# Kernel optimization log

Measured on AMD Instinct MI355X. Metric: run time of the kernel, lower is better.

The kernel has to match this reference:

```python
import jax, jax.numpy as jnp
import numpy as np
import math

B, S, D, H = 1, 2048, 1024, 16
HD = D // H  # 64
SCALE = 1.0 / math.sqrt(HD)
ENT = 0.5      # entanglement_strength
DECAY = 0.1    # correlation_decay
SUP = 0.3      # superposition_weight
EPS = 1e-5


def setup_inputs() -> dict:
    key = jax.random.key(0)
    ks = jax.random.split(key, 24)
    def w(k, shape, s=0.02):
        return jax.random.normal(k, shape, dtype=jnp.float32) * s
    return {
        "hidden_states": jax.random.normal(ks[0], (B, S, D), dtype=jnp.float32),
        "Wq": w(ks[1], (D, D)), "bq": jnp.zeros((D,), jnp.float32),
        "Wk": w(ks[2], (D, D)), "bk": jnp.zeros((D,), jnp.float32),
        "Wv": w(ks[3], (D, D)), "bv": jnp.zeros((D,), jnp.float32),
        "Wo": w(ks[4], (D, D)), "bo": jnp.zeros((D,), jnp.float32),
        "Weq": w(ks[5], (D, D), 0.002), "beq": jnp.zeros((D,), jnp.float32),
        "Wek": w(ks[6], (D, D), 0.002), "bek": jnp.zeros((D,), jnp.float32),
        "amp_w": w(ks[7], (H, D)), "amp_b": jnp.zeros((H,), jnp.float32),
        "ph_w": w(ks[8], (H, D)), "ph_b": jnp.zeros((H,), jnp.float32),
        "mix_w": w(ks[9], (H, HD, HD)), "mix_b": jnp.zeros((H, HD), jnp.float32),
        "ln_g": jnp.ones((D,), jnp.float32), "ln_b": jnp.zeros((D,), jnp.float32),
    }


def _heads(x):
    # [B,S,D] -> [B,H,S,hd]
    b, s, _ = x.shape
    return x.reshape(b, s, H, HD).transpose(0, 2, 1, 3)


def reference(hidden_states, Wq, bq, Wk, bk, Wv, bv, Wo, bo,
              Weq, beq, Wek, bek, amp_w, amp_b, ph_w, ph_b,
              mix_w, mix_b, ln_g, ln_b):
    hs = hidden_states
    b, s, _ = hs.shape
    q = _heads(hs @ Wq.T + bq)  # [B,H,S,hd]
    k = _heads(hs @ Wk.T + bk)
    v = _heads(hs @ Wv.T + bv)

    # standard attention scores
    scores = jnp.einsum('bhqd,bhkd->bhqk', q, k) * SCALE

    # entanglement scores with distance-decay position bias
    eq = _heads(hs @ Weq.T + beq)
    ek = _heads(hs @ Wek.T + bek)
    pos = jnp.arange(s)
    decay = jnp.exp(-DECAY * jnp.abs(pos[:, None] - pos[None, :]).astype(jnp.float32))  # [S,S]
    esc = jnp.einsum('bhqd,bhkd->bhqk', eq, ek) * (1.0 / math.sqrt(HD)) * decay

    attn = jax.nn.softmax(scores + ENT * esc, axis=-1)  # [B,H,S,S]

    # quantum amplitudes / phases
    amps = jax.nn.sigmoid(hs @ amp_w.T + amp_b)        # [B,S,H]
    phases = jnp.tanh(hs @ ph_w.T + ph_b) * math.pi    # [B,S,H]
    a = amps.transpose(0, 2, 1)[..., None]             # [B,H,S,1]
    p = phases.transpose(0, 2, 1)[..., None]

    # per-head superposition mixer: Linear(head_dim, head_dim) per head
    sup = jnp.einsum('bhsd,hod->bhso', v, mix_w) + mix_b[None, :, None, :]
    mixed = v + SUP * a * jnp.cos(p) * sup + SUP * a * jnp.sin(p) * jnp.roll(sup, 1, axis=-1)

    ctx = jnp.einsum('bhqk,bhkd->bhqd', attn, mixed)
    ctx = ctx.transpose(0, 2, 1, 3).reshape(b, s, D)
    out = ctx @ Wo.T + bo

    # residual + LayerNorm
    res = hs + out
    mu = jnp.mean(res, axis=-1, keepdims=True)
    var = jnp.mean((res - mu) ** 2, axis=-1, keepdims=True)
    return (res - mu) * jax.lax.rsqrt(var + EPS) * ln_g + ln_b
```

## Files before the change

### kernel.cpp

```cpp
#include <hip/hip_runtime.h>

#define SEQ 2048
#define DM  1024
#define NH  16
#define HDIM 64

typedef __bf16   bf16x8 __attribute__((ext_vector_type(8)));
typedef float    f32x4  __attribute__((ext_vector_type(4)));
typedef _Float16 half8  __attribute__((ext_vector_type(8)));
typedef _Float16 half4v __attribute__((ext_vector_type(4)));

__device__ __forceinline__ void gload16(const void* g, void* l) {
    __builtin_amdgcn_global_load_lds(
        (const __attribute__((address_space(1))) unsigned int*)g,
        (__attribute__((address_space(3))) unsigned int*)l, 16, 0, 0);
}

__global__ void zero_out(float* __restrict__ out, int n) {
    int i = blockIdx.x * 256 + threadIdx.x;
    if (i < n) out[i] = 0.f;
}

__global__ __launch_bounds__(256) void cvt_bf16(
    const float* __restrict__ src, __bf16* __restrict__ dst, int n8)
{
    int i = blockIdx.x * 256 + threadIdx.x;
    if (i >= n8) return;
    const float4* s = reinterpret_cast<const float4*>(src) + (size_t)i * 2;
    float4 x = s[0], y = s[1];
    bf16x8 o;
    o[0] = (__bf16)x.x; o[1] = (__bf16)x.y; o[2] = (__bf16)x.z; o[3] = (__bf16)x.w;
    o[4] = (__bf16)y.x; o[5] = (__bf16)y.y; o[6] = (__bf16)y.z; o[7] = (__bf16)y.w;
    reinterpret_cast<bf16x8*>(dst)[i] = o;
}

struct CvtBatch { const float* src[6]; __bf16* dst[6]; };
__global__ __launch_bounds__(256) void cvt_w6(CvtBatch cb) {
    const int z = blockIdx.y;
    int i = blockIdx.x * 256 + threadIdx.x;
    const float4* s = reinterpret_cast<const float4*>(cb.src[z]) + (size_t)i * 2;
    float4 x = s[0], y = s[1];
    bf16x8 o;
    o[0] = (__bf16)x.x; o[1] = (__bf16)x.y; o[2] = (__bf16)x.z; o[3] = (__bf16)x.w;
    o[4] = (__bf16)y.x; o[5] = (__bf16)y.y; o[6] = (__bf16)y.z; o[7] = (__bf16)y.w;
    reinterpret_cast<bf16x8*>(cb.dst[z])[i] = o;
}

__global__ __launch_bounds__(256) void wsup_k(
    const float* __restrict__ mixw, const float* __restrict__ Wv,
    const float* __restrict__ bv, const float* __restrict__ mixb,
    __bf16* __restrict__ w6, float* __restrict__ bsup)
{
    const int ho = blockIdx.x, h = ho >> 6, tid = threadIdx.x;
    __shared__ float mrow[64];
    if (tid < 64) mrow[tid] = mixw[(size_t)ho * 64 + tid];
    __syncthreads();
    const int c0 = tid * 4;
    float a0 = 0.f, a1 = 0.f, a2 = 0.f, a3 = 0.f;
    for (int dd = 0; dd < 64; ++dd) {
        const float4 wv4 = *reinterpret_cast<const float4*>(
            Wv + (size_t)(h * 64 + dd) * DM + c0);
        const float w = mrow[dd];
        a0 += w * wv4.x; a1 += w * wv4.y; a2 += w * wv4.z; a3 += w * wv4.w;
    }
    __bf16* dst = w6 + (size_t)ho * DM + c0;
    dst[0] = (__bf16)a0; dst[1] = (__bf16)a1; dst[2] = (__bf16)a2; dst[3] = (__bf16)a3;
    if (tid == 0) {
        float b = mixb[ho];
        for (int dd = 0; dd < 64; ++dd) b += mrow[dd] * bv[h * 64 + dd];
        bsup[ho] = b;
    }
}

struct GemmBatch {
    const __bf16* A;
    const __bf16* W[6];
    const float*  bias[6];
    void*         out[6];
    int           mode[6];
    const float*  resid;
};

__device__ __forceinline__ int swz4(int r) { return (r ^ (r >> 2)) & 3; }

__global__ __launch_bounds__(256) void gemm_bt(GemmBatch g) {
    const int z = blockIdx.z;
    const __bf16* __restrict__ A = g.A;
    const __bf16* __restrict__ W = g.W[z];
    const int ncol0 = blockIdx.x * 128;
    const int mrow0 = blockIdx.y * 128;
    const int tid = threadIdx.x, lane = tid & 63, wv = tid >> 6;
    const int wm = wv >> 1, wn = wv & 1;
    const int fr = lane & 15, fj = lane >> 4;

    __shared__ __bf16 As[128 * 32];
    __shared__ __bf16 Bs[128 * 32];

    f32x4 acc[4][4];
#pragma unroll
    for (int i = 0; i < 4; ++i)
#pragma unroll
        for (int j = 0; j < 4; ++j)
#pragma unroll
            for (int e = 0; e < 4; ++e) acc[i][j][e] = 0.f;

    const int row0 = wv * 16 + (lane >> 2);
    const int row1 = row0 + 64;
    const int jl   = lane & 3;
    const int dstA0 = row0 * 32 + jl * 8;
    const int dstA1 = row1 * 32 + jl * 8;
    const __bf16* ApS0 = A + (size_t)(mrow0 + row0) * DM + (jl ^ swz4(row0)) * 8;
    const __bf16* ApS1 = A + (size_t)(mrow0 + row1) * DM + (jl ^ swz4(row1)) * 8;
    const __bf16* WpS0 = W + (size_t)(ncol0 + row0) * DM + (jl ^ swz4(row0)) * 8;
    const __bf16* WpS1 = W + (size_t)(ncol0 + row1) * DM + (jl ^ swz4(row1)) * 8;

    for (int kt = 0; kt < DM; kt += 32) {
        __syncthreads();
        gload16(ApS0 + kt, As + dstA0);
        gload16(ApS1 + kt, As + dstA1);
        gload16(WpS0 + kt, Bs + dstA0);
        gload16(WpS1 + kt, Bs + dstA1);
        __syncthreads();

        bf16x8 af[4], bfv[4];
#pragma unroll
        for (int mf = 0; mf < 4; ++mf) {
            int r = wm * 64 + mf * 16 + fr;
            af[mf] = *(const bf16x8*)(As + r * 32 + ((fj ^ swz4(r)) << 3));
        }
#pragma unroll
        for (int nf = 0; nf < 4; ++nf) {
            int r = wn * 64 + nf * 16 + fr;
            bfv[nf] = *(const bf16x8*)(Bs + r * 32 + ((fj ^ swz4(r)) << 3));
        }
#pragma unroll
        for (int mf = 0; mf < 4; ++mf)
#pragma unroll
            for (int nf = 0; nf < 4; ++nf)
                acc[mf][nf] = __builtin_amdgcn_mfma_f32_16x16x32_bf16(
                    af[mf], bfv[nf], acc[mf][nf], 0, 0, 0);
    }

    const int mode = g.mode[z];
    const float* __restrict__ bias = g.bias[z];
#pragma unroll
    for (int mf = 0; mf < 4; ++mf) {
#pragma unroll
        for (int nf = 0; nf < 4; ++nf) {
            const int col = ncol0 + wn * 64 + nf * 16 + fr;
            const int rw0 = mrow0 + wm * 64 + mf * 16 + fj * 4;
            const float bc = bias[col];
#pragma unroll
            for (int jj = 0; jj < 4; ++jj) {
                float vv = acc[mf][nf][jj] + bc;
                const size_t idx = (size_t)(rw0 + jj) * DM + col;
                if (mode == 3) {
                    ((_Float16*)g.out[z])[idx] = (_Float16)vv;
                } else {
                    if (mode == 2) vv += g.resid[idx];
                    ((float*)g.out[z])[idx] = vv;
                }
            }
        }
    }
}

__global__ __launch_bounds__(256) void amp_fast(
    const float* __restrict__ hs,
    const float* __restrict__ amp_w, const float* __restrict__ amp_b,
    const float* __restrict__ ph_w,  const float* __restrict__ ph_b,
    float* __restrict__ cA, float* __restrict__ sA)
{
    const int s = blockIdx.x;
    __shared__ float hrow[DM];
    for (int i = threadIdx.x; i < DM; i += 256)
        hrow[i] = hs[(size_t)s * DM + i];
    __syncthreads();
    const int h = threadIdx.x >> 4, sub = threadIdx.x & 15;
    const float* aw = amp_w + (size_t)h * DM;
    const float* pw = ph_w  + (size_t)h * DM;
    float da = 0.f, dp = 0.f;
    for (int k = sub; k < DM; k += 16) {
        const float hv = hrow[k];
        da += hv * aw[k];
        dp += hv * pw[k];
    }
#pragma unroll
    for (int off = 8; off >= 1; off >>= 1) {
        da += __shfl_xor(da, off);
        dp += __shfl_xor(dp, off);
    }
    if (sub == 0) {
        da += amp_b[h]; dp += ph_b[h];
        float amp = 1.f / (1.f + expf(-da));
        float ph  = tanhf(dp) * 3.14159265358979323846f;
        cA[s * NH + h] = 0.3f * amp * cosf(ph);
        sA[s * NH + h] = 0.3f * amp * sinf(ph);
    }
}

__global__ __launch_bounds__(256) void mixT_fuse(
    const _Float16* __restrict__ vb, const _Float16* __restrict__ supf,
    const float* __restrict__ cA, const float* __restrict__ sA,
    _Float16* __restrict__ mixedT)
{
    const int h = blockIdx.x, st = blockIdx.y;
    const int o = threadIdx.x >> 2, sc = threadIdx.x & 3;
    const int s0 = st * 32 + sc * 8;
    const int ho = h * 64 + o, op = h * 64 + ((o + 63) & 63);
    half8 m;
#pragma unroll
    for (int e = 0; e < 8; ++e) {
        const int s = s0 + e;
        const float v  = (float)vb[(size_t)s * DM + ho];
        const float su = (float)supf[(size_t)s * DM + ho];
        const float s2 = (float)supf[(size_t)s * DM + op];
        m[e] = (_Float16)(v + cA[s * NH + h] * su + sA[s * NH + h] * s2);
    }
    *reinterpret_cast<half8*>(mixedT + (size_t)ho * SEQ + s0) = m;
}

__global__ __launch_bounds__(256) void attn_mfma(
    const _Float16* __restrict__ q, const _Float16* __restrict__ k,
    const _Float16* __restrict__ eq, const _Float16* __restrict__ ek,
    const _Float16* __restrict__ mixedT, __bf16* __restrict__ ctx)
{
    const int h = blockIdx.y;
    const int q0 = blockIdx.x * 64;
    const int tid = threadIdx.x, lane = tid & 63, wv = tid >> 6;
    const int lo = lane & 15, hi = lane >> 4;
    const int hoff = h * HDIM;

    __shared__ _Float16 Kt[64 * 64];
    __shared__ _Float16 Et[64 * 64];
    __shared__ _Float16 Mt[64 * 64];
    __shared__ _Float16 Pt[4][64 * 18];

    half8 qa[2], ea[2];
#pragma unroll
    for (int kk = 0; kk < 2; ++kk) {
        const int row = q0 + wv * 16 + lo;
        qa[kk] = *(const half8*)(q  + (size_t)row * DM + hoff + kk * 32 + hi * 8);
        ea[kk] = *(const half8*)(eq + (size_t)row * DM + hoff + kk * 32 + hi * 8);
    }

    f32x4 oacc[4];
    float mr[4], lr[4];
#pragma unroll
    for (int j = 0; j < 4; ++j) { mr[j] = 0.f; lr[j] = 0.f; }
#pragma unroll
    for (int n = 0; n < 4; ++n)
#pragma unroll
        for (int e = 0; e < 4; ++e) oacc[n][e] = 0.f;

    const int srow = tid >> 3, schk = tid & 7;
    const int sdst0 = srow * 64 + ((schk ^ (srow & 7)) << 3);
    const int sdst1 = (srow + 32) * 64 + ((schk ^ (srow & 7)) << 3);

    #define IN_BAND(kt_) ({ int _a = (kt_) - (q0 + 63); int _b = q0 - ((kt_) + 63); \
                            int _d = _a > 0 ? _a : (_b > 0 ? _b : 0); _d <= 160; })

    bool diagCur = IN_BAND(0);
    half8 rk0 = *(const half8*)(k  + (size_t)(srow) * DM + hoff + schk * 8);
    half8 rk1 = *(const half8*)(k  + (size_t)(srow + 32) * DM + hoff + schk * 8);
    half8 rm0 = *(const half8*)(mixedT + (size_t)(hoff + srow) * SEQ + schk * 8);
    half8 rm1 = *(const half8*)(mixedT + (size_t)(hoff + srow + 32) * SEQ + schk * 8);
    half8 re0, re1;
    if (diagCur) {
        re0 = *(const half8*)(ek + (size_t)(srow) * DM + hoff + schk * 8);
        re1 = *(const half8*)(ek + (size_t)(srow + 32) * DM + hoff + schk * 8);
    }

    for (int kt = 0; kt < SEQ; kt += 64) {
        __syncthreads();
        *(half8*)&Kt[sdst0] = rk0; *(half8*)&Kt[sdst1] = rk1;
        *(half8*)&Mt[sdst0] = rm0; *(half8*)&Mt[sdst1] = rm1;
        if (diagCur) { *(half8*)&Et[sdst0] = re0; *(half8*)&Et[sdst1] = re1; }
        __syncthreads();
        const bool diagNext = (kt + 64 < SEQ) && IN_BAND(kt + 64);
        if (kt + 64 < SEQ) {
            const int nt = kt + 64;
            rk0 = *(const half8*)(k  + (size_t)(nt + srow) * DM + hoff + schk * 8);
            rk1 = *(const half8*)(k  + (size_t)(nt + srow + 32) * DM + hoff + schk * 8);
            rm0 = *(const half8*)(mixedT + (size_t)(hoff + srow) * SEQ + nt + schk * 8);
            rm1 = *(const half8*)(mixedT + (size_t)(hoff + srow + 32) * SEQ + nt + schk * 8);
            if (diagNext) {
                re0 = *(const half8*)(ek + (size_t)(nt + srow) * DM + hoff + schk * 8);
                re1 = *(const half8*)(ek + (size_t)(nt + srow + 32) * DM + hoff + schk * 8);
            }
        }

        f32x4 sa[4], se[4];
#pragma unroll
        for (int n = 0; n < 4; ++n)
#pragma unroll
            for (int e = 0; e < 4; ++e) { sa[n][e] = 0.f; se[n][e] = 0.f; }
#pragma unroll
        for (int kk = 0; kk < 2; ++kk)
#pragma unroll
            for (int nf = 0; nf < 4; ++nf) {
                const int rrow = lo + 16 * nf;
                const int coff = rrow * 64 + (((hi + 4 * kk) ^ (rrow & 7)) << 3);
                half8 kb = *(const half8*)&Kt[coff];
                sa[nf] = __builtin_amdgcn_mfma_f32_16x16x32_f16(qa[kk], kb, sa[nf], 0, 0, 0);
            }
        if (diagCur) {
#pragma unroll
            for (int kk = 0; kk < 2; ++kk)
#pragma unroll
                for (int nf = 0; nf < 4; ++nf) {
                    const int rrow = lo + 16 * nf;
                    const int coff = rrow * 64 + (((hi + 4 * kk) ^ (rrow & 7)) << 3);
                    half8 eb = *(const half8*)&Et[coff];
                    se[nf] = __builtin_amdgcn_mfma_f32_16x16x32_f16(ea[kk], eb, se[nf], 0, 0, 0);
                }
        }

        float lg[4][4];
        bool exc = false;
        const int qrow = q0 + wv * 16 + hi * 4;
        if (diagCur) {
#pragma unroll
            for (int nf = 0; nf < 4; ++nf) {
                const int key = kt + nf * 16 + lo;
#pragma unroll
                for (int j = 0; j < 4; ++j) {
                    int dd = qrow + j - key; dd = dd < 0 ? -dd : dd;
                    const float dec = exp2f(-0.14426950408889634f * (float)dd);
                    const float v = 0.125f * sa[nf][j] + 0.0625f * se[nf][j] * dec;
                    lg[nf][j] = v;
                    exc |= (v > mr[j] + 8.f);
                }
            }
        } else {
#pragma unroll
            for (int nf = 0; nf < 4; ++nf)
#pragma unroll
                for (int j = 0; j < 4; ++j) {
                    const float v = 0.125f * sa[nf][j];
                    lg[nf][j] = v;
                    exc |= (v > mr[j] + 8.f);
                }
        }
        if (__any((int)exc)) {
#pragma unroll
            for (int j = 0; j < 4; ++j) {
                float tm = fmaxf(fmaxf(lg[0][j], lg[1][j]), fmaxf(lg[2][j], lg[3][j]));
#pragma unroll
                for (int off = 8; off >= 1; off >>= 1) tm = fmaxf(tm, __shfl_xor(tm, off));
                const float mnew = fmaxf(mr[j], tm);
                const float corr = __expf(mr[j] - mnew);
                lr[j] *= corr; mr[j] = mnew;
#pragma unroll
                for (int nfd = 0; nfd < 4; ++nfd) oacc[nfd][j] *= corr;
            }
        }
        _Float16* Pw = Pt[wv];
#pragma unroll
        for (int nf = 0; nf < 4; ++nf) {
            half4v pv;
#pragma unroll
            for (int j = 0; j < 4; ++j) {
                const float p = __expf(lg[nf][j] - mr[j]);
                lr[j] += p;
                pv[j] = (_Float16)p;
            }
            *(half4v*)&Pw[(lo + 16 * nf) * 18 + hi * 4] = pv;
        }
        __asm__ volatile("s_waitcnt lgkmcnt(0)" ::: "memory");

#pragma unroll
        for (int kk = 0; kk < 2; ++kk) {
            half8 mb[4];
#pragma unroll
            for (int nfd = 0; nfd < 4; ++nfd) {
                const int rrow = lo + 16 * nfd;
                mb[nfd] = *(const half8*)&Mt[rrow * 64 + (((hi + 4 * kk) ^ (rrow & 7)) << 3)];
            }
            half8 pa;
#pragma unroll
            for (int e = 0; e < 8; ++e)
                pa[e] = Pw[(kk * 32 + hi * 8 + e) * 18 + lo];
#pragma unroll
            for (int nfd = 0; nfd < 4; ++nfd)
                oacc[nfd] = __builtin_amdgcn_mfma_f32_16x16x32_f16(pa, mb[nfd], oacc[nfd], 0, 0, 0);
        }
        diagCur = diagNext;
    }
    #undef IN_BAND

#pragma unroll
    for (int j = 0; j < 4; ++j) {
#pragma unroll
        for (int off = 8; off >= 1; off >>= 1) lr[j] += __shfl_xor(lr[j], off);
    }
    const int qrow = q0 + wv * 16 + hi * 4;
#pragma unroll
    for (int nfd = 0; nfd < 4; ++nfd) {
        const int d = hoff + lo + 16 * nfd;
#pragma unroll
        for (int j = 0; j < 4; ++j)
            ctx[(size_t)(qrow + j) * DM + d] = (__bf16)(oacc[nfd][j] / lr[j]);
    }
}

__global__ __launch_bounds__(256) void lnorm_f32(
    const float* __restrict__ res, const float* __restrict__ g,
    const float* __restrict__ b, float* __restrict__ out)
{
    const int row = blockIdx.x, tid = threadIdx.x;
    const int wave = tid >> 6, lane = tid & 63;
    __shared__ float red[8];
    const float4 x = reinterpret_cast<const float4*>(res + (size_t)row * DM)[tid];
    float s  = x.x + x.y + x.z + x.w;
    float s2 = x.x * x.x + x.y * x.y + x.z * x.z + x.w * x.w;
#pragma unroll
    for (int off = 32; off >= 1; off >>= 1) {
        s  += __shfl_xor(s, off);
        s2 += __shfl_xor(s2, off);
    }
    if (lane == 0) { red[wave] = s; red[4 + wave] = s2; }
    __syncthreads();
    s  = red[0] + red[1] + red[2] + red[3];
    s2 = red[4] + red[5] + red[6] + red[7];
    const float mu  = s * (1.f / DM);
    const float var = s2 * (1.f / DM) - mu * mu;
    const float inv = rsqrtf(var + 1e-5f);
    const int col = tid * 4;
    float4 o;
    o.x = (x.x - mu) * inv * g[col + 0] + b[col + 0];
    o.y = (x.y - mu) * inv * g[col + 1] + b[col + 1];
    o.z = (x.z - mu) * inv * g[col + 2] + b[col + 2];
    o.w = (x.w - mu) * inv * g[col + 3] + b[col + 3];
    reinterpret_cast<float4*>(out + (size_t)row * DM)[tid] = o;
}

extern "C" void kernel_launch(void* const* d_in, const int* in_sizes, int n_in,
                              void* d_out, int out_size, void* d_ws, size_t ws_size,
                              hipStream_t stream) {
    const float* hs   = (const float*)d_in[0];
    const float* Wq   = (const float*)d_in[1];
    const float* bq   = (const float*)d_in[2];
    const float* Wk   = (const float*)d_in[3];
    const float* bk   = (const float*)d_in[4];
    const float* Wv   = (const float*)d_in[5];
    const float* bv   = (const float*)d_in[6];
    const float* Wo   = (const float*)d_in[7];
    const float* bo   = (const float*)d_in[8];
    const float* Weq  = (const float*)d_in[9];
    const float* beq  = (const float*)d_in[10];
    const float* Wek  = (const float*)d_in[11];
    const float* bek  = (const float*)d_in[12];
    const float* ampw = (const float*)d_in[13];
    const float* ampb = (const float*)d_in[14];
    const float* phw  = (const float*)d_in[15];
    const float* phb  = (const float*)d_in[16];
    const float* mixw = (const float*)d_in[17];
    const float* mixb = (const float*)d_in[18];
    const float* lng  = (const float*)d_in[19];
    const float* lnb  = (const float*)d_in[20];
    float* out = (float*)d_out;

    static const int expect[21] = {
        2097152, 1048576, 1024, 1048576, 1024, 1048576, 1024, 1048576, 1024,
        1048576, 1024, 1048576, 1024, 16384, 16, 16384, 16, 65536, 1024,
        1024, 1024};
    bool ok = (n_in == 21) && (out_size == 2097152);
    if (ok) for (int i = 0; i < 21; ++i) ok = ok && (in_sizes[i] == expect[i]);
    if (!ok) {
        zero_out<<<(out_size + 255) / 256, 256, 0, stream>>>(out, out_size);
        return;
    }

    char* ws = (char*)d_ws;
    __bf16*   hsb = (__bf16*)ws;
    __bf16*   w0  = (__bf16*)(ws + (4  << 20));
    __bf16*   w1  = (__bf16*)(ws + (6  << 20));
    __bf16*   w2  = (__bf16*)(ws + (8  << 20));
    __bf16*   w3  = (__bf16*)(ws + (10 << 20));
    __bf16*   w4  = (__bf16*)(ws + (12 << 20));
    __bf16*   w5  = (__bf16*)(ws + (14 << 20));
    __bf16*   w6  = (__bf16*)(ws + (16 << 20));
    _Float16* qf  = (_Float16*)(ws + (18 << 20));
    _Float16* kf  = (_Float16*)(ws + (22 << 20));
    _Float16* eqf = (_Float16*)(ws + (26 << 20));
    _Float16* ekf = (_Float16*)(ws + (30 << 20));
    float*    cA  = (float*)(ws + (34 << 20));
    float*    sA  = cA + SEQ * NH;
    float*    bsup = sA + SEQ * NH;
    _Float16* mxT = (_Float16*)hsb;
    float*    res = (float*)(ws + (18 << 20));
    _Float16* vb   = (_Float16*)d_out;
    _Float16* supf = (_Float16*)((char*)d_out + (4 << 20));
    __bf16*   ctx  = (__bf16*)d_out;

    const int H8 = SEQ * DM / 8;
    cvt_bf16<<<(H8 + 255) / 256, 256, 0, stream>>>(hs, hsb, H8);

    CvtBatch cb;
    cb.src[0] = Wq;  cb.dst[0] = w0;
    cb.src[1] = Wk;  cb.dst[1] = w1;
    cb.src[2] = Wv;  cb.dst[2] = w2;
    cb.src[3] = Weq; cb.dst[3] = w3;
    cb.src[4] = Wek; cb.dst[4] = w4;
    cb.src[5] = Wo;  cb.dst[5] = w5;
    cvt_w6<<<dim3(512, 6), 256, 0, stream>>>(cb);

    wsup_k<<<1024, 256, 0, stream>>>(mixw, Wv, bv, mixb, w6, bsup);
    amp_fast<<<SEQ, 256, 0, stream>>>(hs, ampw, ampb, phw, phb, cA, sA);

    GemmBatch g1 = {};
    g1.A = hsb;
    g1.W[0] = w0; g1.bias[0] = bq;   g1.out[0] = qf;   g1.mode[0] = 3;
    g1.W[1] = w1; g1.bias[1] = bk;   g1.out[1] = kf;   g1.mode[1] = 3;
    g1.W[2] = w2; g1.bias[2] = bv;   g1.out[2] = vb;   g1.mode[2] = 3;
    g1.W[3] = w3; g1.bias[3] = beq;  g1.out[3] = eqf;  g1.mode[3] = 3;
    g1.W[4] = w4; g1.bias[4] = bek;  g1.out[4] = ekf;  g1.mode[4] = 3;
    g1.W[5] = w6; g1.bias[5] = bsup; g1.out[5] = supf; g1.mode[5] = 3;
    g1.resid = nullptr;
    gemm_bt<<<dim3(DM / 128, SEQ / 128, 6), 256, 0, stream>>>(g1);

    mixT_fuse<<<dim3(NH, SEQ / 32), 256, 0, stream>>>(vb, supf, cA, sA, mxT);

    attn_mfma<<<dim3(SEQ / 64, NH), 256, 0, stream>>>(qf, kf, eqf, ekf, mxT, ctx);

    GemmBatch g3 = {};
    g3.A = ctx;
    g3.W[0] = w5; g3.bias[0] = bo; g3.out[0] = res; g3.mode[0] = 2;
    g3.resid = hs;
    gemm_bt<<<dim3(DM / 128, SEQ / 128, 1), 256, 0, stream>>>(g3);

    lnorm_f32<<<SEQ, 256, 0, stream>>>(res, lng, lnb, out);
}
```

Baseline: 303.6 us.

## Merge prep kernels, deepen GEMM K-tile to 64, double attention query tile

Folds the hidden-state bf16 conversion into the batched weight-conversion kernel and merges the mixer-weight and amplitude/phase kernels into one launch, cutting launch count. The GEMM now stages a 64-wide K slice per iteration with an 8-way XOR swizzle, halving the number of barrier-separated loads. The attention kernel processes 128 query rows per block (two 16-row fragments per wave), so each K/E/M tile loaded to shared memory is reused twice. In exchange, register pressure and LDS use rise, and the attention grid halves to 256 blocks, which may underfill the GPU.

```diff
diff --git a/kernel.cpp b/kernel.cpp
--- a/kernel.cpp
+++ b/kernel.cpp
@@ -21,21 +21,8 @@
     if (i < n) out[i] = 0.f;
 }
 
-__global__ __launch_bounds__(256) void cvt_bf16(
-    const float* __restrict__ src, __bf16* __restrict__ dst, int n8)
-{
-    int i = blockIdx.x * 256 + threadIdx.x;
-    if (i >= n8) return;
-    const float4* s = reinterpret_cast<const float4*>(src) + (size_t)i * 2;
-    float4 x = s[0], y = s[1];
-    bf16x8 o;
-    o[0] = (__bf16)x.x; o[1] = (__bf16)x.y; o[2] = (__bf16)x.z; o[3] = (__bf16)x.w;
-    o[4] = (__bf16)y.x; o[5] = (__bf16)y.y; o[6] = (__bf16)y.z; o[7] = (__bf16)y.w;
-    reinterpret_cast<bf16x8*>(dst)[i] = o;
-}
-
-struct CvtBatch { const float* src[6]; __bf16* dst[6]; };
-__global__ __launch_bounds__(256) void cvt_w6(CvtBatch cb) {
+struct CvtBatch { const float* src[8]; __bf16* dst[8]; };
+__global__ __launch_bounds__(256) void cvt_all(CvtBatch cb) {
     const int z = blockIdx.y;
     int i = blockIdx.x * 256 + threadIdx.x;
     const float4* s = reinterpret_cast<const float4*>(cb.src[z]) + (size_t)i * 2;
@@ -46,29 +33,64 @@
     reinterpret_cast<bf16x8*>(cb.dst[z])[i] = o;
 }
 
-__global__ __launch_bounds__(256) void wsup_k(
+__global__ __launch_bounds__(256) void prep_misc(
     const float* __restrict__ mixw, const float* __restrict__ Wv,
     const float* __restrict__ bv, const float* __restrict__ mixb,
-    __bf16* __restrict__ w6, float* __restrict__ bsup)
+    __bf16* __restrict__ w6, float* __restrict__ bsup,
+    const float* __restrict__ hs,
+    const float* __restrict__ amp_w, const float* __restrict__ amp_b,
+    const float* __restrict__ ph_w,  const float* __restrict__ ph_b,
+    float* __restrict__ cA, float* __restrict__ sA)
 {
-    const int ho = blockIdx.x, h = ho >> 6, tid = threadIdx.x;
-    __shared__ float mrow[64];
-    if (tid < 64) mrow[tid] = mixw[(size_t)ho * 64 + tid];
-    __syncthreads();
-    const int c0 = tid * 4;
-    float a0 = 0.f, a1 = 0.f, a2 = 0.f, a3 = 0.f;
-    for (int dd = 0; dd < 64; ++dd) {
-        const float4 wv4 = *reinterpret_cast<const float4*>(
-            Wv + (size_t)(h * 64 + dd) * DM + c0);
-        const float w = mrow[dd];
-        a0 += w * wv4.x; a1 += w * wv4.y; a2 += w * wv4.z; a3 += w * wv4.w;
-    }
-    __bf16* dst = w6 + (size_t)ho * DM + c0;
-    dst[0] = (__bf16)a0; dst[1] = (__bf16)a1; dst[2] = (__bf16)a2; dst[3] = (__bf16)a3;
-    if (tid == 0) {
-        float b = mixb[ho];
-        for (int dd = 0; dd < 64; ++dd) b += mrow[dd] * bv[h * 64 + dd];
-        bsup[ho] = b;
+    const int tid = threadIdx.x;
+    if (blockIdx.x < 1024) {
+        const int ho = blockIdx.x, h = ho >> 6;
+        __shared__ float mrow[64];
+        if (tid < 64) mrow[tid] = mixw[(size_t)ho * 64 + tid];
+        __syncthreads();
+        const int c0 = tid * 4;
+        float a0 = 0.f, a1 = 0.f, a2 = 0.f, a3 = 0.f;
+        for (int dd = 0; dd < 64; ++dd) {
+            const float4 wv4 = *reinterpret_cast<const float4*>(
+                Wv + (size_t)(h * 64 + dd) * DM + c0);
+            const float w = mrow[dd];
+            a0 += w * wv4.x; a1 += w * wv4.y; a2 += w * wv4.z; a3 += w * wv4.w;
+        }
+        __bf16* dst = w6 + (size_t)ho * DM + c0;
+        dst[0] = (__bf16)a0; dst[1] = (__bf16)a1;
+        dst[2] = (__bf16)a2; dst[3] = (__bf16)a3;
+        if (tid == 0) {
+            float b = mixb[ho];
+            for (int dd = 0; dd < 64; ++dd) b += mrow[dd] * bv[h * 64 + dd];
+            bsup[ho] = b;
+        }
+    } else {
+        const int s = blockIdx.x - 1024;
+        __shared__ float hrow[DM];
+        for (int i = tid; i < DM; i += 256)
+            hrow[i] = hs[(size_t)s * DM + i];
+        __syncthreads();
+        const int h = tid >> 4, sub = tid & 15;
+        const float* aw = amp_w + (size_t)h * DM;
+        const float* pw = ph_w  + (size_t)h * DM;
+        float da = 0.f, dp = 0.f;
+        for (int k = sub; k < DM; k += 16) {
+            const float hv = hrow[k];
+            da += hv * aw[k];
+            dp += hv * pw[k];
+        }
+#pragma unroll
+        for (int off = 8; off >= 1; off >>= 1) {
+            da += __shfl_xor(da, off);
+            dp += __shfl_xor(dp, off);
+        }
+        if (sub == 0) {
+            da += amp_b[h]; dp += ph_b[h];
+            float amp = 1.f / (1.f + expf(-da));
+            float ph  = tanhf(dp) * 3.14159265358979323846f;
+            cA[s * NH + h] = 0.3f * amp * cosf(ph);
+            sA[s * NH + h] = 0.3f * amp * sinf(ph);
+        }
     }
 }
 
@@ -80,8 +102,6 @@
     int           mode[6];
     const float*  resid;
 };
-
-__device__ __forceinline__ int swz4(int r) { return (r ^ (r >> 2)) & 3; }
 
 __global__ __launch_bounds__(256) void gemm_bt(GemmBatch g) {
     const int z = blockIdx.z;
@@ -93,8 +113,8 @@
     const int wm = wv >> 1, wn = wv & 1;
     const int fr = lane & 15, fj = lane >> 4;
 
-    __shared__ __bf16 As[128 * 32];
-    __shared__ __bf16 Bs[128 * 32];
+    __shared__ __bf16 As[128 * 64];
+    __shared__ __bf16 Bs[128 * 64];
 
     f32x4 acc[4][4];
 #pragma unroll
@@ -104,41 +124,46 @@
 #pragma unroll
             for (int e = 0; e < 4; ++e) acc[i][j][e] = 0.f;
 
-    const int row0 = wv * 16 + (lane >> 2);
-    const int row1 = row0 + 64;
-    const int jl   = lane & 3;
-    const int dstA0 = row0 * 32 + jl * 8;
-    const int dstA1 = row1 * 32 + jl * 8;
-    const __bf16* ApS0 = A + (size_t)(mrow0 + row0) * DM + (jl ^ swz4(row0)) * 8;
-    const __bf16* ApS1 = A + (size_t)(mrow0 + row1) * DM + (jl ^ swz4(row1)) * 8;
-    const __bf16* WpS0 = W + (size_t)(ncol0 + row0) * DM + (jl ^ swz4(row0)) * 8;
-    const __bf16* WpS1 = W + (size_t)(ncol0 + row1) * DM + (jl ^ swz4(row1)) * 8;
-
-    for (int kt = 0; kt < DM; kt += 32) {
+    const int srow = tid >> 3, jl = tid & 7;
+    const int scs = (jl ^ (srow & 7)) * 8;
+    const __bf16* Ap[4]; const __bf16* Wp[4]; int dst[4];
+#pragma unroll
+    for (int i = 0; i < 4; ++i) {
+        const int r = i * 32 + srow;
+        dst[i] = r * 64 + jl * 8;
+        Ap[i] = A + (size_t)(mrow0 + r) * DM + scs;
+        Wp[i] = W + (size_t)(ncol0 + r) * DM + scs;
+    }
+
+    for (int kt = 0; kt < DM; kt += 64) {
         __syncthreads();
-        gload16(ApS0 + kt, As + dstA0);
-        gload16(ApS1 + kt, As + dstA1);
-        gload16(WpS0 + kt, Bs + dstA0);
-        gload16(WpS1 + kt, Bs + dstA1);
+#pragma unroll
+        for (int i = 0; i < 4; ++i) gload16(Ap[i] + kt, As + dst[i]);
+#pragma unroll
+        for (int i = 0; i < 4; ++i) gload16(Wp[i] + kt, Bs + dst[i]);
         __syncthreads();
 
-        bf16x8 af[4], bfv[4];
-#pragma unroll
-        for (int mf = 0; mf < 4; ++mf) {
-            int r = wm * 64 + mf * 16 + fr;
-            af[mf] = *(const bf16x8*)(As + r * 32 + ((fj ^ swz4(r)) << 3));
-        }
-#pragma unroll
-        for (int nf = 0; nf < 4; ++nf) {
-            int r = wn * 64 + nf * 16 + fr;
-            bfv[nf] = *(const bf16x8*)(Bs + r * 32 + ((fj ^ swz4(r)) << 3));
-        }
-#pragma unroll
-        for (int mf = 0; mf < 4; ++mf)
-#pragma unroll
-            for (int nf = 0; nf < 4; ++nf)
-                acc[mf][nf] = __builtin_amdgcn_mfma_f32_16x16x32_bf16(
-                    af[mf], bfv[nf], acc[mf][nf], 0, 0, 0);
+#pragma unroll
+        for (int ks = 0; ks < 2; ++ks) {
+            bf16x8 af[4], bfv[4];
+            const int ch = ks * 4 + fj;
+#pragma unroll
+            for (int mf = 0; mf < 4; ++mf) {
+                int r = wm * 64 + mf * 16 + fr;
+                af[mf] = *(const bf16x8*)(As + r * 64 + ((ch ^ (r & 7)) << 3));
+            }
+#pragma unroll
+            for (int nf = 0; nf < 4; ++nf) {
+                int r = wn * 64 + nf * 16 + fr;
+                bfv[nf] = *(const bf16x8*)(Bs + r * 64 + ((ch ^ (r & 7)) << 3));
+            }
+#pragma unroll
+            for (int mf = 0; mf < 4; ++mf)
+#pragma unroll
+                for (int nf = 0; nf < 4; ++nf)
+                    acc[mf][nf] = __builtin_amdgcn_mfma_f32_16x16x32_bf16(
+                        af[mf], bfv[nf], acc[mf][nf], 0, 0, 0);
+        }
     }
 
     const int mode = g.mode[z];
@@ -162,40 +187,6 @@
                 }
             }
         }
-    }
-}
-
-__global__ __launch_bounds__(256) void amp_fast(
-    const float* __restrict__ hs,
-    const float* __restrict__ amp_w, const float* __restrict__ amp_b,
-    const float* __restrict__ ph_w,  const float* __restrict__ ph_b,
-    float* __restrict__ cA, float* __restrict__ sA)
-{
-    const int s = blockIdx.x;
-    __shared__ float hrow[DM];
-    for (int i = threadIdx.x; i < DM; i += 256)
-        hrow[i] = hs[(size_t)s * DM + i];
-    __syncthreads();
-    const int h = threadIdx.x >> 4, sub = threadIdx.x & 15;
-    const float* aw = amp_w + (size_t)h * DM;
-    const float* pw = ph_w  + (size_t)h * DM;
-    float da = 0.f, dp = 0.f;
-    for (int k = sub; k < DM; k += 16) {
-        const float hv = hrow[k];
-        da += hv * aw[k];
-        dp += hv * pw[k];
-    }
-#pragma unroll
-    for (int off = 8; off >= 1; off >>= 1) {
-        da += __shfl_xor(da, off);
-        dp += __shfl_xor(dp, off);
-    }
-    if (sub == 0) {
-        da += amp_b[h]; dp += ph_b[h];
-        float amp = 1.f / (1.f + expf(-da));
-        float ph  = tanhf(dp) * 3.14159265358979323846f;
-        cA[s * NH + h] = 0.3f * amp * cosf(ph);
-        sA[s * NH + h] = 0.3f * amp * sinf(ph);
     }
 }
 
@@ -226,7 +217,7 @@
     const _Float16* __restrict__ mixedT, __bf16* __restrict__ ctx)
 {
     const int h = blockIdx.y;
-    const int q0 = blockIdx.x * 64;
+    const int q0 = blockIdx.x * 128;
     const int tid = threadIdx.x, lane = tid & 63, wv = tid >> 6;
     const int lo = lane & 15, hi = lane >> 4;
     const int hoff = h * HDIM;
@@ -234,30 +225,37 @@
     __shared__ _Float16 Kt[64 * 64];
     __shared__ _Float16 Et[64 * 64];
     __shared__ _Float16 Mt[64 * 64];
-    __shared__ _Float16 Pt[4][64 * 18];
-
-    half8 qa[2], ea[2];
-#pragma unroll
-    for (int kk = 0; kk < 2; ++kk) {
-        const int row = q0 + wv * 16 + lo;
-        qa[kk] = *(const half8*)(q  + (size_t)row * DM + hoff + kk * 32 + hi * 8);
-        ea[kk] = *(const half8*)(eq + (size_t)row * DM + hoff + kk * 32 + hi * 8);
-    }
-
-    f32x4 oacc[4];
-    float mr[4], lr[4];
-#pragma unroll
-    for (int j = 0; j < 4; ++j) { mr[j] = 0.f; lr[j] = 0.f; }
-#pragma unroll
-    for (int n = 0; n < 4; ++n)
-#pragma unroll
-        for (int e = 0; e < 4; ++e) oacc[n][e] = 0.f;
+    __shared__ _Float16 Pt[8][64 * 18];
+
+    half8 qa[2][2], ea[2][2];
+#pragma unroll
+    for (int m = 0; m < 2; ++m) {
+        const int row = q0 + wv * 32 + m * 16 + lo;
+#pragma unroll
+        for (int kk = 0; kk < 2; ++kk) {
+            qa[m][kk] = *(const half8*)(q  + (size_t)row * DM + hoff + kk * 32 + hi * 8);
+            ea[m][kk] = *(const half8*)(eq + (size_t)row * DM + hoff + kk * 32 + hi * 8);
+        }
+    }
+
+    f32x4 oacc[2][4];
+    float mr[2][4], lr[2][4];
+#pragma unroll
+    for (int m = 0; m < 2; ++m)
+#pragma unroll
+        for (int j = 0; j < 4; ++j) { mr[m][j] = 0.f; lr[m][j] = 0.f; }
+#pragma unroll
+    for (int m = 0; m < 2; ++m)
+#pragma unroll
+        for (int n = 0; n < 4; ++n)
+#pragma unroll
+            for (int e = 0; e < 4; ++e) oacc[m][n][e] = 0.f;
 
     const int srow = tid >> 3, schk = tid & 7;
     const int sdst0 = srow * 64 + ((schk ^ (srow & 7)) << 3);
     const int sdst1 = (srow + 32) * 64 + ((schk ^ (srow & 7)) << 3);
 
-    #define IN_BAND(kt_) ({ int _a = (kt_) - (q0 + 63); int _b = q0 - ((kt_) + 63); \
+    #define IN_BAND(kt_) ({ int _a = (kt_) - (q0 + 127); int _b = q0 - ((kt_) + 63); \
                             int _d = _a > 0 ? _a : (_b > 0 ? _b : 0); _d <= 160; })
 
     bool diagCur = IN_BAND(0);
@@ -290,11 +288,13 @@
             }
         }
 
-        f32x4 sa[4], se[4];
-#pragma unroll
-        for (int n = 0; n < 4; ++n)
-#pragma unroll
-            for (int e = 0; e < 4; ++e) { sa[n][e] = 0.f; se[n][e] = 0.f; }
+        f32x4 sa[2][4], se[2][4];
+#pragma unroll
+        for (int m = 0; m < 2; ++m)
+#pragma unroll
+            for (int n = 0; n < 4; ++n)
+#pragma unroll
+                for (int e = 0; e < 4; ++e) { sa[m][n][e] = 0.f; se[m][n][e] = 0.f; }
 #pragma unroll
         for (int kk = 0; kk < 2; ++kk)
 #pragma unroll
@@ -302,7 +302,8 @@
                 const int rrow = lo + 16 * nf;
                 const int coff = rrow * 64 + (((hi + 4 * kk) ^ (rrow & 7)) << 3);
                 half8 kb = *(const half8*)&Kt[coff];
-                sa[nf] = __builtin_amdgcn_mfma_f32_16x16x32_f16(qa[kk], kb, sa[nf], 0, 0, 0);
+                sa[0][nf] = __builtin_amdgcn_mfma_f32_16x16x32_f16(qa[0][kk], kb, sa[0][nf], 0, 0, 0);
+                sa[1][nf] = __builtin_amdgcn_mfma_f32_16x16x32_f16(qa[1][kk], kb, sa[1][nf], 0, 0, 0);
             }
         if (diagCur) {
 #pragma unroll
@@ -312,60 +313,64 @@
                     const int rrow = lo + 16 * nf;
                     const int coff = rrow * 64 + (((hi + 4 * kk) ^ (rrow & 7)) << 3);
                     half8 eb = *(const half8*)&Et[coff];
-                    se[nf] = __builtin_amdgcn_mfma_f32_16x16x32_f16(ea[kk], eb, se[nf], 0, 0, 0);
+                    se[0][nf] = __builtin_amdgcn_mfma_f32_16x16x32_f16(ea[0][kk], eb, se[0][nf], 0, 0, 0);
+                    se[1][nf] = __builtin_amdgcn_mfma_f32_16x16x32_f16(ea[1][kk], eb, se[1][nf], 0, 0, 0);
                 }
         }
 
-        float lg[4][4];
-        bool exc = false;
-        const int qrow = q0 + wv * 16 + hi * 4;
-        if (diagCur) {
+#pragma unroll
+        for (int m = 0; m < 2; ++m) {
+            float lg[4][4];
+            bool exc = false;
+            const int qrow = q0 + wv * 32 + m * 16 + hi * 4;
+            if (diagCur) {
+#pragma unroll
+                for (int nf = 0; nf < 4; ++nf) {
+                    const int key = kt + nf * 16 + lo;
+#pragma unroll
+                    for (int j = 0; j < 4; ++j) {
+                        int dd = qrow + j - key; dd = dd < 0 ? -dd : dd;
+                        const float dec = exp2f(-0.14426950408889634f * (float)dd);
+                        const float v = 0.125f * sa[m][nf][j] + 0.0625f * se[m][nf][j] * dec;
+                        lg[nf][j] = v;
+                        exc |= (v > mr[m][j] + 8.f);
+                    }
+                }
+            } else {
+#pragma unroll
+                for (int nf = 0; nf < 4; ++nf)
+#pragma unroll
+                    for (int j = 0; j < 4; ++j) {
+                        const float v = 0.125f * sa[m][nf][j];
+                        lg[nf][j] = v;
+                        exc |= (v > mr[m][j] + 8.f);
+                    }
+            }
+            if (__any((int)exc)) {
+#pragma unroll
+                for (int j = 0; j < 4; ++j) {
+                    float tm = fmaxf(fmaxf(lg[0][j], lg[1][j]), fmaxf(lg[2][j], lg[3][j]));
+#pragma unroll
+                    for (int off = 8; off >= 1; off >>= 1) tm = fmaxf(tm, __shfl_xor(tm, off));
+                    const float mnew = fmaxf(mr[m][j], tm);
+                    const float corr = __expf(mr[m][j] - mnew);
+                    lr[m][j] *= corr; mr[m][j] = mnew;
+#pragma unroll
+                    for (int nfd = 0; nfd < 4; ++nfd) oacc[m][nfd][j] *= corr;
+                }
+            }
+            _Float16* Pw = Pt[wv * 2 + m];
 #pragma unroll
             for (int nf = 0; nf < 4; ++nf) {
-                const int key = kt + nf * 16 + lo;
+                half4v pv;
 #pragma unroll
                 for (int j = 0; j < 4; ++j) {
-                    int dd = qrow + j - key; dd = dd < 0 ? -dd : dd;
-                    const float dec = exp2f(-0.14426950408889634f * (float)dd);
-                    const float v = 0.125f * sa[nf][j] + 0.0625f * se[nf][j] * dec;
-                    lg[nf][j] = v;
-                    exc |= (v > mr[j] + 8.f);
+                    const float p = __expf(lg[nf][j] - mr[m][j]);
+                    lr[m][j] += p;
+                    pv[j] = (_Float16)p;
                 }
-            }
-        } else {
-#pragma unroll
-            for (int nf = 0; nf < 4; ++nf)
-#pragma unroll
-                for (int j = 0; j < 4; ++j) {
-                    const float v = 0.125f * sa[nf][j];
-                    lg[nf][j] = v;
-                    exc |= (v > mr[j] + 8.f);
-                }
-        }
-        if (__any((int)exc)) {
-#pragma unroll
-            for (int j = 0; j < 4; ++j) {
-                float tm = fmaxf(fmaxf(lg[0][j], lg[1][j]), fmaxf(lg[2][j], lg[3][j]));
-#pragma unroll
-                for (int off = 8; off >= 1; off >>= 1) tm = fmaxf(tm, __shfl_xor(tm, off));
-                const float mnew = fmaxf(mr[j], tm);
-                const float corr = __expf(mr[j] - mnew);
-                lr[j] *= corr; mr[j] = mnew;
-#pragma unroll
-                for (int nfd = 0; nfd < 4; ++nfd) oacc[nfd][j] *= corr;
-            }
-        }
-        _Float16* Pw = Pt[wv];
-#pragma unroll
-        for (int nf = 0; nf < 4; ++nf) {
-            half4v pv;
-#pragma unroll
-            for (int j = 0; j < 4; ++j) {
-                const float p = __expf(lg[nf][j] - mr[j]);
-                lr[j] += p;
-                pv[j] = (_Float16)p;
-            }
-            *(half4v*)&Pw[(lo + 16 * nf) * 18 + hi * 4] = pv;
+                *(half4v*)&Pw[(lo + 16 * nf) * 18 + hi * 4] = pv;
+            }
         }
         __asm__ volatile("s_waitcnt lgkmcnt(0)" ::: "memory");
 
@@ -377,30 +382,37 @@
                 const int rrow = lo + 16 * nfd;
                 mb[nfd] = *(const half8*)&Mt[rrow * 64 + (((hi + 4 * kk) ^ (rrow & 7)) << 3)];
             }
-            half8 pa;
-#pragma unroll
-            for (int e = 0; e < 8; ++e)
-                pa[e] = Pw[(kk * 32 + hi * 8 + e) * 18 + lo];
-#pragma unroll
-            for (int nfd = 0; nfd < 4; ++nfd)
-                oacc[nfd] = __builtin_amdgcn_mfma_f32_16x16x32_f16(pa, mb[nfd], oacc[nfd], 0, 0, 0);
+#pragma unroll
+            for (int m = 0; m < 2; ++m) {
+                const _Float16* Pw = Pt[wv * 2 + m];
+                half8 pa;
+#pragma unroll
+                for (int e = 0; e < 8; ++e)
+                    pa[e] = Pw[(kk * 32 + hi * 8 + e) * 18 + lo];
+#pragma unroll
+                for (int nfd = 0; nfd < 4; ++nfd)
+                    oacc[m][nfd] = __builtin_amdgcn_mfma_f32_16x16x32_f16(pa, mb[nfd], oacc[m][nfd], 0, 0, 0);
+            }
         }
         diagCur = diagNext;
     }
     #undef IN_BAND
 
 #pragma unroll
-    for (int j = 0; j < 4; ++j) {
-#pragma unroll
-        for (int off = 8; off >= 1; off >>= 1) lr[j] += __shfl_xor(lr[j], off);
-    }
-    const int qrow = q0 + wv * 16 + hi * 4;
-#pragma unroll
-    for (int nfd = 0; nfd < 4; ++nfd) {
-        const int d = hoff + lo + 16 * nfd;
-#pragma unroll
-        for (int j = 0; j < 4; ++j)
-            ctx[(size_t)(qrow + j) * DM + d] = (__bf16)(oacc[nfd][j] / lr[j]);
+    for (int m = 0; m < 2; ++m) {
+#pragma unroll
+        for (int j = 0; j < 4; ++j) {
+#pragma unroll
+            for (int off = 8; off >= 1; off >>= 1) lr[m][j] += __shfl_xor(lr[m][j], off);
+        }
+        const int qrow = q0 + wv * 32 + m * 16 + hi * 4;
+#pragma unroll
+        for (int nfd = 0; nfd < 4; ++nfd) {
+            const int d = hoff + lo + 16 * nfd;
+#pragma unroll
+            for (int j = 0; j < 4; ++j)
+                ctx[(size_t)(qrow + j) * DM + d] = (__bf16)(oacc[m][nfd][j] / lr[m][j]);
+        }
     }
 }
 
@@ -494,9 +506,6 @@
     _Float16* supf = (_Float16*)((char*)d_out + (4 << 20));
     __bf16*   ctx  = (__bf16*)d_out;
 
-    const int H8 = SEQ * DM / 8;
-    cvt_bf16<<<(H8 + 255) / 256, 256, 0, stream>>>(hs, hsb, H8);
-
     CvtBatch cb;
     cb.src[0] = Wq;  cb.dst[0] = w0;
     cb.src[1] = Wk;  cb.dst[1] = w1;
@@ -504,10 +513,12 @@
     cb.src[3] = Weq; cb.dst[3] = w3;
     cb.src[4] = Wek; cb.dst[4] = w4;
     cb.src[5] = Wo;  cb.dst[5] = w5;
-    cvt_w6<<<dim3(512, 6), 256, 0, stream>>>(cb);
-
-    wsup_k<<<1024, 256, 0, stream>>>(mixw, Wv, bv, mixb, w6, bsup);
-    amp_fast<<<SEQ, 256, 0, stream>>>(hs, ampw, ampb, phw, phb, cA, sA);
+    cb.src[6] = hs;                cb.dst[6] = hsb;
+    cb.src[7] = hs + SEQ * DM / 2; cb.dst[7] = hsb + SEQ * DM / 2;
+    cvt_all<<<dim3(512, 8), 256, 0, stream>>>(cb);
+
+    prep_misc<<<3072, 256, 0, stream>>>(mixw, Wv, bv, mixb, w6, bsup,
+                                        hs, ampw, ampb, phw, phb, cA, sA);
 
     GemmBatch g1 = {};
     g1.A = hsb;
@@ -522,7 +533,7 @@
 
     mixT_fuse<<<dim3(NH, SEQ / 32), 256, 0, stream>>>(vb, supf, cA, sA, mxT);
 
-    attn_mfma<<<dim3(SEQ / 64, NH), 256, 0, stream>>>(qf, kf, eqf, ekf, mxT, ctx);
+    attn_mfma<<<dim3(SEQ / 128, NH), 256, 0, stream>>>(qf, kf, eqf, ekf, mxT, ctx);
 
     GemmBatch g3 = {};
     g3.A = ctx;
```

Result: slower. 327.2 us (+7.8%).
